# Optimization experiments

Measured on AMD Instinct MI355X. Metric: run time of the kernel, lower is better.

The kernel has to match this reference:

```python
import jax, jax.numpy as jnp
import numpy as np

B, T, E = 4, 2048, 256
H = 8
HD = E // H
FE = 4
L = 4
EPS = 1e-5


def _layernorm(x, g, b):
    mu = jnp.mean(x, axis=-1, keepdims=True)
    var = jnp.mean((x - mu) ** 2, axis=-1, keepdims=True)
    return (x - mu) * jax.lax.rsqrt(var + EPS) * g + b


def setup_inputs() -> dict:
    key = jax.random.key(0)
    ks = jax.random.split(key, 14)
    s = 0.02
    inp = {
        "x": jax.random.normal(ks[0], (B, T, E), dtype=jnp.float32),
        "qkv_w": jax.random.normal(ks[1], (L, E, 3 * E), dtype=jnp.float32) * s,
        "qkv_b": jnp.zeros((L, 3 * E), jnp.float32),
        "out_w": jax.random.normal(ks[2], (L, E, E), dtype=jnp.float32) * s,
        "out_b": jnp.zeros((L, E), jnp.float32),
        "ff1_w": jax.random.normal(ks[3], (L, E, FE * E), dtype=jnp.float32) * s,
        "ff1_b": jnp.zeros((L, FE * E), jnp.float32),
        "ff2_w": jax.random.normal(ks[4], (L, FE * E, E), dtype=jnp.float32) * s,
        "ff2_b": jnp.zeros((L, E), jnp.float32),
        "ln1_g": jnp.ones((L, E), jnp.float32),
        "ln1_b": jnp.zeros((L, E), jnp.float32),
        "ln2_g": jnp.ones((L, E), jnp.float32),
        "ln2_b": jnp.zeros((L, E), jnp.float32),
    }
    return inp


def _fourier_pe(x):
    # freqs over even indices: 10000^(-i/E), i = 0,2,...,E-2  -> E/2 freqs
    freqs = jnp.power(10000.0, -jnp.arange(0, E, 2, dtype=jnp.float32) / E)
    pos = jnp.arange(T, dtype=jnp.float32)[:, None]          # (T,1)
    sinusoid = pos * freqs[None, :]                            # (T, E/2)
    pe = jnp.concatenate([jnp.sin(sinusoid), jnp.cos(sinusoid)], axis=-1)  # (T,E)
    return x + pe[None, :, :]


def _forward(x, qkv_w, qkv_b, out_w, out_b, ff1_w, ff1_b, ff2_w, ff2_b,
             ln1_g, ln1_b, ln2_g, ln2_b):
    x = _fourier_pe(x)
    scale = 1.0 / np.sqrt(HD)
    for i in range(L):
        # attention (dropout = identity at eval)
        qkv = x @ qkv_w[i] + qkv_b[i]                          # (B,T,3E)
        qkv = qkv.reshape(B, T, H, 3, HD)                      # chunk of 3*hd -> (3,hd)
        q, k, v = qkv[..., 0, :], qkv[..., 1, :], qkv[..., 2, :]  # (B,T,H,HD)
        scores = jnp.einsum("bqhd,bkhd->bhqk", q, k) * scale   # (B,H,T,T)
        w = jax.nn.softmax(scores, axis=-1)
        attn = jnp.einsum("bhqk,bkhd->bqhd", w, v).reshape(B, T, E)
        attn = attn @ out_w[i] + out_b[i]
        x = _layernorm(x + attn, ln1_g[i], ln1_b[i])
        # feedforward
        h = jax.nn.relu(x @ ff1_w[i] + ff1_b[i])
        ff = h @ ff2_w[i] + ff2_b[i]
        x = _layernorm(x + ff, ln2_g[i], ln2_b[i])
    return x


def reference(x, qkv_w, qkv_b, out_w, out_b, ff1_w, ff1_b, ff2_w, ff2_b,
              ln1_g, ln1_b, ln2_g, ln2_b):
    return _forward(x, qkv_w, qkv_b, out_w, out_b, ff1_w, ff1_b, ff2_w, ff2_b,
                    ln1_g, ln1_b, ln2_g, ln2_b)
```

## Files before the change

### kernel.cpp

```cpp
#include <hip/hip_runtime.h>
#include <hip/hip_bf16.h>
#include <stdint.h>

typedef unsigned short u16;
typedef _Float16 f16;
typedef short vs8 __attribute__((ext_vector_type(8)));
typedef float vf4 __attribute__((ext_vector_type(4)));
typedef _Float16 vh2 __attribute__((ext_vector_type(2)));
typedef _Float16 vh4 __attribute__((ext_vector_type(4)));
typedef _Float16 vh8 __attribute__((ext_vector_type(8)));
typedef __fp16 hw2 __attribute__((ext_vector_type(2)));



__device__ __forceinline__ void gload16(const u16* g, u16* l) {
  __builtin_amdgcn_global_load_lds((const __attribute__((address_space(1))) void*)g,
                                   (__attribute__((address_space(3))) void*)l,
                                   16, 0, 0);
}

__device__ __forceinline__ float fexp2(float x) {
#if __has_builtin(__builtin_amdgcn_exp2f)
  return __builtin_amdgcn_exp2f(x);
#else
  return __expf(x * 0.69314718056f);
#endif
}

__global__ void pe_kernel(const float* __restrict__ x, __hip_bfloat16* __restrict__ Xb) {
  int gid = blockIdx.x * 256 + threadIdx.x;
  int row = gid >> 6;
  int e0 = (gid & 63) * 4;
  int t = row & 2047;
  int f0 = (e0 < 128) ? e0 : (e0 - 128);
  const float c = -13.287712379549449f / 128.0f;
  const float inv2pi = 0.15915494309189535f;
  float4 xv = *(const float4*)(x + (size_t)row * 256 + e0);
  u16 o[4];
#pragma unroll
  for (int j = 0; j < 4; ++j) {
    float freq = fexp2(c * (float)(f0 + j));
    float rev = (float)t * freq * inv2pi;
    rev = rev - floorf(rev);
    float pe = (e0 < 128) ? __builtin_amdgcn_sinf(rev) : __builtin_amdgcn_cosf(rev);
    float xin = (j == 0) ? xv.x : (j == 1) ? xv.y : (j == 2) ? xv.z : xv.w;
    __hip_bfloat16 hb = __float2bfloat16(xin + pe);
    o[j] = *(u16*)&hb;
  }
  *(uint2*)((u16*)Xb + (size_t)row * 256 + e0) = *(uint2*)o;
}

__global__ void transpose_cast_all(
    const float* __restrict__ w0, const float* __restrict__ w1,
    const float* __restrict__ w2, const float* __restrict__ w3,
    u16* __restrict__ o0, u16* __restrict__ o1,
    u16* __restrict__ o2, u16* __restrict__ o3) {
  __shared__ float tile[32][33];
  int flat = blockIdx.x;
  int layer = flat / 768;
  int r = flat - layer * 768;
  const float* ip; u16* op; int K, N, kt, nt;
  if (r < 192)      {              ip = w0; op = o0; K = 256;  N = 768;  kt = r & 7;  nt = r >> 3; }
  else if (r < 256) { int q=r-192; ip = w1; op = o1; K = 256;  N = 256;  kt = q & 7;  nt = q >> 3; }
  else if (r < 512) { int q=r-256; ip = w2; op = o2; K = 256;  N = 1024; kt = q & 7;  nt = q >> 3; }
  else              { int q=r-512; ip = w3; op = o3; K = 1024; N = 256;  kt = q & 31; nt = q >> 5; }
  ip += (size_t)layer * K * N;
  op += (size_t)layer * N * K;
  int k0 = kt * 32, n0 = nt * 32;
  int tx = threadIdx.x, ty = threadIdx.y;
#pragma unroll
  for (int rr = 0; rr < 4; ++rr) {
    int k = ty + rr * 8;
    tile[k][tx] = ip[(size_t)(k0 + k) * N + (n0 + tx)];
  }
  __syncthreads();
#pragma unroll
  for (int rr = 0; rr < 4; ++rr) {
    int n = ty + rr * 8;
    __hip_bfloat16 v = __float2bfloat16(tile[tx][n]);
    op[(size_t)(n0 + n) * K + (k0 + tx)] = *(u16*)&v;
  }
}

__global__ __launch_bounds__(256, 2) void gemm_relu(
    const u16* __restrict__ A, const u16* __restrict__ Bt,
    const float* __restrict__ bias, __hip_bfloat16* __restrict__ outB,
    int M, int N, int K) {
  __shared__ u16 As[128 * 64];
  __shared__ u16 Bs[128 * 64];
  int tid = threadIdx.x;
  int wave = tid >> 6, lane = tid & 63;
  int wm = wave & 1, wn = wave >> 1;
  int m0 = blockIdx.y * 128, n0 = blockIdx.x * 128;
  int lr = lane & 15, lq = lane >> 4;
  int swz = (lr & 7) << 3;

  vf4 acc[4][4];
#pragma unroll
  for (int i = 0; i < 4; ++i)
#pragma unroll
    for (int j = 0; j < 4; ++j) {
      acc[i][j][0] = 0.f; acc[i][j][1] = 0.f; acc[i][j][2] = 0.f; acc[i][j][3] = 0.f;
    }

  int srow = tid >> 3;
  int sc = (tid & 7) * 8;
  int cswz = (((tid & 7) ^ (srow & 7)) * 8);
  const u16* ag = A + (size_t)(m0 + srow) * K + cswz;
  const u16* bg = Bt + (size_t)(n0 + srow) * K + cswz;
  u16* al = As + srow * 64 + sc;
  u16* bl = Bs + srow * 64 + sc;
  const size_t rstride32 = (size_t)32 * K;

  for (int k0 = 0; k0 < K; k0 += 64) {
#pragma unroll
    for (int r = 0; r < 4; ++r) {
      gload16(ag + k0 + r * rstride32, al + r * 32 * 64);
      gload16(bg + k0 + r * rstride32, bl + r * 32 * 64);
    }
    __syncthreads();
#pragma unroll
    for (int kk = 0; kk < 2; ++kk) {
      vs8 av[4], bv[4];
#pragma unroll
      for (int i = 0; i < 4; ++i)
        av[i] = *(const vs8*)&As[(wm * 64 + i * 16 + lr) * 64 + ((kk * 32 + lq * 8) ^ swz)];
#pragma unroll
      for (int j = 0; j < 4; ++j)
        bv[j] = *(const vs8*)&Bs[(wn * 64 + j * 16 + lr) * 64 + ((kk * 32 + lq * 8) ^ swz)];
#pragma unroll
      for (int i = 0; i < 4; ++i)
#pragma unroll
        for (int j = 0; j < 4; ++j)
          acc[i][j] = __builtin_amdgcn_mfma_f32_16x16x32_bf16(av[i], bv[j], acc[i][j], 0, 0, 0);
    }
    __syncthreads();
  }

#pragma unroll
  for (int i = 0; i < 4; ++i) {
    int row0 = m0 + wm * 64 + i * 16 + lq * 4;
#pragma unroll
    for (int j = 0; j < 4; ++j) {
      int col = n0 + wn * 64 + j * 16 + lr;
      float bb = bias[col];
#pragma unroll
      for (int r = 0; r < 4; ++r) {
        size_t idx = (size_t)(row0 + r) * N + col;
        outB[idx] = __float2bfloat16(fmaxf(acc[i][j][r] + bb, 0.0f));
      }
    }
  }
}

__global__ __launch_bounds__(256, 3) void gemm_qkv64(
    const u16* __restrict__ A, const u16* __restrict__ Bt,
    const float* __restrict__ bias, f16* __restrict__ outH,
    int M, int N, int K) {
  __shared__ u16 As[64 * 64];
  __shared__ u16 Bs[128 * 64];
  int tid = threadIdx.x;
  int wave = tid >> 6, lane = tid & 63;
  int wm = wave & 1, wn = wave >> 1;
  int m0 = blockIdx.y * 64, n0 = blockIdx.x * 128;
  int lr = lane & 15, lq = lane >> 4;
  int swz = (lr & 7) << 3;

  vf4 acc[2][4];
#pragma unroll
  for (int i = 0; i < 2; ++i)
#pragma unroll
    for (int j = 0; j < 4; ++j) { acc[i][j][0]=0.f; acc[i][j][1]=0.f; acc[i][j][2]=0.f; acc[i][j][3]=0.f; }

  int srow = tid >> 3;
  int sc = (tid & 7) * 8;
  int cswz = (((tid & 7) ^ (srow & 7)) * 8);
  const u16* ag = A + (size_t)(m0 + srow) * K + cswz;
  const u16* bg = Bt + (size_t)(n0 + srow) * K + cswz;
  u16* al = As + srow * 64 + sc;
  u16* bl = Bs + srow * 64 + sc;
  const size_t rstride32 = (size_t)32 * K;

  for (int k0 = 0; k0 < K; k0 += 64) {
#pragma unroll
    for (int r = 0; r < 2; ++r)
      gload16(ag + k0 + r * rstride32, al + r * 32 * 64);
#pragma unroll
    for (int r = 0; r < 4; ++r)
      gload16(bg + k0 + r * rstride32, bl + r * 32 * 64);
    __syncthreads();
#pragma unroll
    for (int kk = 0; kk < 2; ++kk) {
      vs8 av[2], bv[4];
#pragma unroll
      for (int i = 0; i < 2; ++i)
        av[i] = *(const vs8*)&As[(wm * 32 + i * 16 + lr) * 64 + ((kk * 32 + lq * 8) ^ swz)];
#pragma unroll
      for (int j = 0; j < 4; ++j)
        bv[j] = *(const vs8*)&Bs[(wn * 64 + j * 16 + lr) * 64 + ((kk * 32 + lq * 8) ^ swz)];
#pragma unroll
      for (int i = 0; i < 2; ++i)
#pragma unroll
        for (int j = 0; j < 4; ++j)
          acc[i][j] = __builtin_amdgcn_mfma_f32_16x16x32_bf16(av[i], bv[j], acc[i][j], 0, 0, 0);
    }
    __syncthreads();
  }

#pragma unroll
  for (int i = 0; i < 2; ++i) {
    int row0 = m0 + wm * 32 + i * 16 + lq * 4;
#pragma unroll
    for (int j = 0; j < 4; ++j) {
      int col = n0 + wn * 64 + j * 16 + lr;
      float bb = bias[col];
#pragma unroll
      for (int r = 0; r < 4; ++r)
        outH[(size_t)(row0 + r) * N + col] = (f16)(acc[i][j][r] + bb);
    }
  }
}

__global__ __launch_bounds__(512, 2) void gemm_ln(
    const u16* __restrict__ A, const u16* __restrict__ Bt,
    const float* __restrict__ bias, const __hip_bfloat16* __restrict__ res,
    const float* __restrict__ gam, const float* __restrict__ bet,
    __hip_bfloat16* __restrict__ outB, float* __restrict__ outF, int K,
    const f16* __restrict__ OfA, const float* __restrict__ lf) {
  __shared__ u16 As[32 * 64];
  __shared__ u16 Bs[256 * 64];
  __shared__ float ps[4][32], ps2[4][32], mur[32], rsr[32];
  __shared__ float invs[8][32];
  int tid = threadIdx.x;
  int wave = tid >> 6, lane = tid & 63;
  int wm = wave & 1, wn = wave >> 1;
  int lr = lane & 15, lq = lane >> 4;
  int m0 = blockIdx.x * 32;
  int swz = (lr & 7) << 3;

  vf4 acc[4];
#pragma unroll
  for (int j = 0; j < 4; ++j) { acc[j][0]=0.f; acc[j][1]=0.f; acc[j][2]=0.f; acc[j][3]=0.f; }

  int sr = tid >> 3;
  int sc = (tid & 7) * 8;
  int cswz = (((tid & 7) ^ (sr & 7)) * 8);
  const u16* ag = A + (size_t)(m0 + sr) * K + cswz;
  const u16* bg = Bt + (size_t)sr * K + cswz;
  u16* al = As + sr * 64 + sc;
  u16* bl = Bs + sr * 64 + sc;

  if (OfA) {
    if (tid < 256) {
      int h = tid >> 5, rl = tid & 31;
      int row = m0 + rl, bb_ = row >> 11, t = row & 2047;
      int g = bb_ * 8 + h;
      invs[h][rl] = 1.0f / (lf[g * 2048 + t] + lf[65536 + g * 2048 + t]);
    }
    __syncthreads();
  }

  for (int k0 = 0; k0 < K; k0 += 64) {
    if (tid < 256) {
      if (OfA) {
        size_t off = (size_t)(m0 + sr) * 256 + k0 + cswz;
        vh8 a0 = *(const vh8*)(OfA + off);
        vh8 a1 = *(const vh8*)(OfA + 2097152 + off);
        float inv = invs[(k0 + cswz) >> 5][sr];
        union { vs8 v; u16 u[8]; } pk;
#pragma unroll
        for (int j = 0; j < 8; ++j) {
          __hip_bfloat16 hb = __float2bfloat16(((float)a0[j] + (float)a1[j]) * inv);
          pk.u[j] = *(u16*)&hb;
        }
        *(vs8*)al = pk.v;
      } else {
        gload16(ag + k0, al);
      }
    }
#pragma unroll
    for (int r = 0; r < 4; ++r)
      gload16(bg + k0 + (size_t)(r * 64) * K, bl + r * 64 * 64);
    __syncthreads();
#pragma unroll
    for (int kk = 0; kk < 2; ++kk) {
      vs8 av, bv[4];
      av = *(const vs8*)&As[(wm * 16 + lr) * 64 + ((kk * 32 + lq * 8) ^ swz)];
#pragma unroll
      for (int j = 0; j < 4; ++j)
        bv[j] = *(const vs8*)&Bs[(wn * 64 + j * 16 + lr) * 64 + ((kk * 32 + lq * 8) ^ swz)];
#pragma unroll
      for (int j = 0; j < 4; ++j)
        acc[j] = __builtin_amdgcn_mfma_f32_16x16x32_bf16(av, bv[j], acc[j], 0, 0, 0);
    }
    __syncthreads();
  }

  float sum_[4], sq_[4];
#pragma unroll
  for (int r = 0; r < 4; ++r) { sum_[r] = 0.f; sq_[r] = 0.f; }
#pragma unroll
  for (int j = 0; j < 4; ++j) {
    int col = wn * 64 + j * 16 + lr;
    float bb = bias[col];
#pragma unroll
    for (int r = 0; r < 4; ++r) {
      int row = m0 + wm * 16 + lq * 4 + r;
      float v = acc[j][r] + bb + __bfloat162float(res[(size_t)row * 256 + col]);
      acc[j][r] = v;
      sum_[r] += v;
      sq_[r] += v * v;
    }
  }
#pragma unroll
  for (int r = 0; r < 4; ++r) {
#pragma unroll
    for (int m = 1; m <= 8; m <<= 1) {
      sum_[r] += __shfl_xor(sum_[r], m);
      sq_[r]  += __shfl_xor(sq_[r], m);
    }
  }
  if (lr == 0) {
#pragma unroll
    for (int r = 0; r < 4; ++r) {
      int rl = wm * 16 + lq * 4 + r;
      ps[wn][rl] = sum_[r];
      ps2[wn][rl] = sq_[r];
    }
  }
  __syncthreads();
  if (tid < 32) {
    float s = ps[0][tid] + ps[1][tid] + ps[2][tid] + ps[3][tid];
    float s2 = ps2[0][tid] + ps2[1][tid] + ps2[2][tid] + ps2[3][tid];
    float mu = s * (1.0f / 256.0f);
    float var = s2 * (1.0f / 256.0f) - mu * mu;
    mur[tid] = mu;
    rsr[tid] = rsqrtf(var + 1e-5f);
  }
  __syncthreads();
#pragma unroll
  for (int r = 0; r < 4; ++r) {
    int rl = wm * 16 + lq * 4 + r;
    float mu = mur[rl], rs = rsr[rl];
    int row = m0 + rl;
#pragma unroll
    for (int j = 0; j < 4; ++j) {
      int col = wn * 64 + j * 16 + lr;
      float o = (acc[j][r] - mu) * rs * gam[col] + bet[col];
      size_t idx = (size_t)row * 256 + col;
      outB[idx] = __float2bfloat16(o);
      if (outF) outF[idx] = o;
    }
  }
}

__global__ __launch_bounds__(512, 4) void attn_mfma(const f16* __restrict__ qkv,
                                                    f16* __restrict__ Of,
                                                    float* __restrict__ lf) {
  __shared__ __align__(16) u16 lds[2][9344];
  int tid = threadIdx.x;
  int wave = tid >> 6, lane = tid & 63;
  int lr = lane & 15, quad = lane >> 4;

  int id = blockIdx.x;
  int xcd = id & 7, slot = id >> 3;
  int grp = xcd * 4 + (slot & 3);
  int qt = (slot >> 2) & 7;
  int split = slot >> 5;
  int b = grp >> 3, h = grp & 7;
  int q0 = qt * 256;
  int kv0 = split << 10;
  int rowbase = b * 2048;
  const f16* base_bh = qkv + (size_t)rowbase * 768 + h * 96;

  vh8 qf[2];
#pragma unroll
  for (int nt = 0; nt < 2; ++nt) {
    int qr = q0 + wave * 32 + nt * 16 + lr;
    vh8 t = *(const vh8*)(base_bh + (size_t)qr * 768 + quad * 8);
#pragma unroll
    for (int j = 0; j < 8; ++j) t[j] = t[j] * (f16)0.25508682f;
    qf[nt] = t;
  }

  vf4 O[2][2], lO[2];
#pragma unroll
  for (int a = 0; a < 2; ++a) {
    lO[a][0]=0.f; lO[a][1]=0.f; lO[a][2]=0.f; lO[a][3]=0.f;
#pragma unroll
    for (int d = 0; d < 2; ++d) { O[a][d][0]=0.f; O[a][d][1]=0.f; O[a][d][2]=0.f; O[a][d][3]=0.f; }
  }

  int srK = tid >> 2;
  int scK = (tid & 3) * 8;
  const f16* kg = base_bh + (size_t)(kv0 + srK) * 768 + 32 + scK;
  int kvp = tid >> 3;
  int d4 = (tid & 7) * 4;
  const f16* vg = base_bh + (size_t)(kv0 + kvp * 2) * 768 + 64 + d4;

  const vf4 z4 = {0.f, 0.f, 0.f, 0.f};
  const vh4 onesh = {(f16)1.0f, (f16)1.0f, (f16)1.0f, (f16)1.0f};
  const size_t cstep = (size_t)128 * 768;

  {
    vh8 k0 = *(const vh8*)kg;
    *(vh8*)&lds[0][srK * 40 + scK] = k0;
    vh4 a = *(const vh4*)vg;
    vh4 bb = *(const vh4*)(vg + 768);
    f16* vt0 = (f16*)&lds[0][5120];
#pragma unroll
    for (int i = 0; i < 4; ++i) {
      vh2 pr; pr[0] = a[i]; pr[1] = bb[i];
      *(vh2*)(vt0 + (d4 + i) * 132 + kvp * 2) = pr;
    }
  }
  __syncthreads();

  for (int c = 0; c < 8; ++c) {
    int cur = c & 1;
    const f16* Ks = (const f16*)&lds[cur][0];
    const f16* VT = (const f16*)&lds[cur][5120];

    vh8 kn; vh4 va, vb;
    if (c < 7) {
      kn = *(const vh8*)(kg + (size_t)(c + 1) * cstep);
      const f16* vp = vg + (size_t)(c + 1) * cstep;
      va = *(const vh4*)vp;
      vb = *(const vh4*)(vp + 768);
    }

    __builtin_amdgcn_s_setprio(1);
#pragma unroll
    for (int t16 = 0; t16 < 8; ++t16) {
      vh8 ak = *(const vh8*)&Ks[(t16 * 16 + lr) * 40 + quad * 8];
      vf4 s0 = __builtin_amdgcn_mfma_f32_16x16x32_f16(ak, qf[0], z4, 0, 0, 0);
      vf4 s1 = __builtin_amdgcn_mfma_f32_16x16x32_f16(ak, qf[1], z4, 0, 0, 0);
      vh4 p0, p1;
      ((hw2*)&p0)[0] = __builtin_amdgcn_cvt_pkrtz(fexp2(s0[0]), fexp2(s0[1]));
      ((hw2*)&p0)[1] = __builtin_amdgcn_cvt_pkrtz(fexp2(s0[2]), fexp2(s0[3]));
      ((hw2*)&p1)[0] = __builtin_amdgcn_cvt_pkrtz(fexp2(s1[0]), fexp2(s1[1]));
      ((hw2*)&p1)[1] = __builtin_amdgcn_cvt_pkrtz(fexp2(s1[2]), fexp2(s1[3]));
      vh4 vf0 = *(const vh4*)&VT[(0 * 16 + lr) * 132 + t16 * 16 + quad * 4];
      vh4 vf1 = *(const vh4*)&VT[(1 * 16 + lr) * 132 + t16 * 16 + quad * 4];
      O[0][0] = __builtin_amdgcn_mfma_f32_16x16x16f16(p0, vf0, O[0][0], 0, 0, 0);
      O[0][1] = __builtin_amdgcn_mfma_f32_16x16x16f16(p0, vf1, O[0][1], 0, 0, 0);
      O[1][0] = __builtin_amdgcn_mfma_f32_16x16x16f16(p1, vf0, O[1][0], 0, 0, 0);
      O[1][1] = __builtin_amdgcn_mfma_f32_16x16x16f16(p1, vf1, O[1][1], 0, 0, 0);
      lO[0] = __builtin_amdgcn_mfma_f32_16x16x16f16(p0, onesh, lO[0], 0, 0, 0);
      lO[1] = __builtin_amdgcn_mfma_f32_16x16x16f16(p1, onesh, lO[1], 0, 0, 0);
    }
    __builtin_amdgcn_s_setprio(0);

    if (c < 7) {
      *(vh8*)&lds[cur ^ 1][srK * 40 + scK] = kn;
      f16* vt1 = (f16*)&lds[cur ^ 1][5120];
#pragma unroll
      for (int i = 0; i < 4; ++i) {
        vh2 pr; pr[0] = va[i]; pr[1] = vb[i];
        *(vh2*)(vt1 + (d4 + i) * 132 + kvp * 2) = pr;
      }
    }
    __syncthreads();
  }

#pragma unroll
  for (int nt = 0; nt < 2; ++nt) {
#pragma unroll
    for (int r = 0; r < 4; ++r) {
      int tq = q0 + wave * 32 + nt * 16 + quad * 4 + r;
      if (lr == 0) lf[split * 65536 + grp * 2048 + tq] = lO[nt][r];
      int row = rowbase + tq;
#pragma unroll
      for (int dt = 0; dt < 2; ++dt) {
        int col = h * 32 + dt * 16 + lr;
        Of[(size_t)split * 2097152 + (size_t)row * 256 + col] = (f16)O[nt][dt][r];
      }
    }
  }
}

extern "C" void kernel_launch(void* const* d_in, const int* in_sizes, int n_in,
                              void* d_out, int out_size, void* d_ws, size_t ws_size,
                              hipStream_t stream) {
  (void)in_sizes; (void)n_in; (void)out_size; (void)ws_size;
  const float* x     = (const float*)d_in[0];
  const float* qkv_b = (const float*)d_in[2];
  const float* out_b = (const float*)d_in[4];
  const float* ff1_b = (const float*)d_in[6];
  const float* ff2_b = (const float*)d_in[8];
  const float* ln1_g = (const float*)d_in[9];
  const float* ln1_b = (const float*)d_in[10];
  const float* ln2_g = (const float*)d_in[11];
  const float* ln2_b = (const float*)d_in[12];

  char* ws = (char*)d_ws;
  f16*            Of    = (f16*)(ws + 0);
  __hip_bfloat16* Xb    = (__hip_bfloat16*)(ws + 8388608);
  float*          lf    = (float*)(ws + 12582912);
  f16*            qkvH  = (f16*)(ws + 25165824);
  __hip_bfloat16* hB    = (__hip_bfloat16*)(ws + 20971520);
  u16* qkvwT = (u16*)(ws + 37748736);
  u16* outwT = (u16*)(ws + 39321600);
  u16* ff1wT = (u16*)(ws + 39845888);
  u16* ff2wT = (u16*)(ws + 41943040);

  pe_kernel<<<2048, 256, 0, stream>>>(x, Xb);
  transpose_cast_all<<<3072, dim3(32, 8), 0, stream>>>(
      (const float*)d_in[1], (const float*)d_in[3], (const float*)d_in[5], (const float*)d_in[7],
      qkvwT, outwT, ff1wT, ff2wT);

  for (int l = 0; l < 4; ++l) {
    gemm_qkv64<<<dim3(6, 128), 256, 0, stream>>>((const u16*)Xb, qkvwT + (size_t)l * 768 * 256,
        qkv_b + l * 768, qkvH, 8192, 768, 256);
    attn_mfma<<<512, 512, 0, stream>>>(qkvH, Of, lf);
    gemm_ln<<<256, 512, 0, stream>>>(nullptr, outwT + (size_t)l * 256 * 256,
        out_b + l * 256, Xb, ln1_g + l * 256, ln1_b + l * 256, Xb, nullptr, 256, Of, lf);
    gemm_relu<<<dim3(8, 64), 256, 0, stream>>>((const u16*)Xb, ff1wT + (size_t)l * 1024 * 256,
        ff1_b + l * 1024, hB, 8192, 1024, 256);
    float* lnout = (l == 3) ? (float*)d_out : nullptr;
    gemm_ln<<<256, 512, 0, stream>>>((const u16*)hB, ff2wT + (size_t)l * 256 * 1024,
        ff2_b + l * 256, Xb, ln2_g + l * 256, ln2_b + l * 256, Xb, lnout, 1024, nullptr, nullptr);
  }
}
```

Measured before the change: 401.9 us.

## Double-buffer gemm_ln K-loop with 32-wide stages and register prefetch of A

The gemm_ln K-loop becomes a double-buffered pipeline with 32-wide K stages. The next stage's A and B tiles are issued via global_load_lds, and the attention-output A operand is prefetched into registers two stages ahead, with manual s_waitcnt and raw s_barrier instead of __syncthreads. A new 4-byte LDS load path and a new XOR swizzle for 32-column tiles are added. The aim is to hide global load latency behind MFMA work, at the cost of more barriers per K, fragile hand-written waitcnt counts and smaller MFMA batches per stage.

```diff
diff --git a/kernel.cpp b/kernel.cpp
--- a/kernel.cpp
+++ b/kernel.cpp
@@ -12,11 +12,15 @@
 typedef __fp16 hw2 __attribute__((ext_vector_type(2)));
 
 
-
 __device__ __forceinline__ void gload16(const u16* g, u16* l) {
   __builtin_amdgcn_global_load_lds((const __attribute__((address_space(1))) void*)g,
                                    (__attribute__((address_space(3))) void*)l,
                                    16, 0, 0);
+}
+__device__ __forceinline__ void gload4(const u16* g, u16* l) {
+  __builtin_amdgcn_global_load_lds((const __attribute__((address_space(1))) void*)g,
+                                   (__attribute__((address_space(3))) void*)l,
+                                   4, 0, 0);
 }
 
 __device__ __forceinline__ float fexp2(float x) {
@@ -227,8 +231,8 @@
     const float* __restrict__ gam, const float* __restrict__ bet,
     __hip_bfloat16* __restrict__ outB, float* __restrict__ outF, int K,
     const f16* __restrict__ OfA, const float* __restrict__ lf) {
-  __shared__ u16 As[32 * 64];
-  __shared__ u16 Bs[256 * 64];
+  __shared__ u16 As[2][32 * 32];
+  __shared__ u16 Bs[2][256 * 32];
   __shared__ float ps[4][32], ps2[4][32], mur[32], rsr[32];
   __shared__ float invs[8][32];
   int tid = threadIdx.x;
@@ -236,64 +240,107 @@
   int wm = wave & 1, wn = wave >> 1;
   int lr = lane & 15, lq = lane >> 4;
   int m0 = blockIdx.x * 32;
-  int swz = (lr & 7) << 3;
+  int fsw = (lq * 8) ^ ((lr & 3) << 3);
 
   vf4 acc[4];
 #pragma unroll
   for (int j = 0; j < 4; ++j) { acc[j][0]=0.f; acc[j][1]=0.f; acc[j][2]=0.f; acc[j][3]=0.f; }
 
-  int sr = tid >> 3;
-  int sc = (tid & 7) * 8;
-  int cswz = (((tid & 7) ^ (sr & 7)) * 8);
-  const u16* ag = A + (size_t)(m0 + sr) * K + cswz;
-  const u16* bg = Bt + (size_t)sr * K + cswz;
-  u16* al = As + sr * 64 + sc;
-  u16* bl = Bs + sr * 64 + sc;
+  int sr0 = tid >> 2, g = tid & 3;
+  int colB = g * 8;
+  int colBs = (g ^ (sr0 & 3)) * 8;
+  const u16* bg = Bt + (size_t)sr0 * K + colBs;
+  int rowA = tid >> 4;
+  int colA2 = (tid & 15) * 2;
+  int colAs = colA2 ^ ((rowA & 3) << 3);
+  const u16* ag4 = A + (size_t)(m0 + rowA) * K + colAs;
+  const size_t OfS = 2097152;
 
   if (OfA) {
     if (tid < 256) {
       int h = tid >> 5, rl = tid & 31;
       int row = m0 + rl, bb_ = row >> 11, t = row & 2047;
-      int g = bb_ * 8 + h;
-      invs[h][rl] = 1.0f / (lf[g * 2048 + t] + lf[65536 + g * 2048 + t]);
+      int gg = bb_ * 8 + h;
+      invs[h][rl] = 1.0f / (lf[gg * 2048 + t] + lf[65536 + gg * 2048 + t]);
     }
     __syncthreads();
   }
 
-  for (int k0 = 0; k0 < K; k0 += 64) {
-    if (tid < 256) {
+  int NS = K >> 5;
+  vh8 ra0, ra1;
+
+  if (OfA) {
+    if (tid < 128) {
+      size_t off = (size_t)(m0 + sr0) * 256 + colBs;
+      vh8 a0 = *(const vh8*)(OfA + off);
+      vh8 a1 = *(const vh8*)(OfA + OfS + off);
+      float inv = invs[colBs >> 5][sr0];
+      union { vs8 v; u16 u[8]; } pk;
+#pragma unroll
+      for (int j = 0; j < 8; ++j) {
+        __hip_bfloat16 hb = __float2bfloat16(((float)a0[j] + (float)a1[j]) * inv);
+        pk.u[j] = *(u16*)&hb;
+      }
+      *(vs8*)&As[0][sr0 * 32 + colB] = pk.v;
+    }
+    gload16(bg, &Bs[0][sr0 * 32 + colB]);
+    gload16(bg + (size_t)128 * K, &Bs[0][(sr0 + 128) * 32 + colB]);
+    if (tid < 128 && NS > 1) {
+      size_t off = (size_t)(m0 + sr0) * 256 + 32 + colBs;
+      ra0 = *(const vh8*)(OfA + off);
+      ra1 = *(const vh8*)(OfA + OfS + off);
+    }
+    asm volatile("s_waitcnt lgkmcnt(0)" ::: "memory");
+  } else {
+    gload4(ag4, &As[0][tid * 2]);
+    gload16(bg, &Bs[0][sr0 * 32 + colB]);
+    gload16(bg + (size_t)128 * K, &Bs[0][(sr0 + 128) * 32 + colB]);
+  }
+
+  for (int s = 0; s < NS; ++s) {
+    int cur = s & 1;
+    if (s + 1 < NS) {
+      int k1 = (s + 1) << 5;
+      u16* bl = &Bs[cur ^ 1][sr0 * 32 + colB];
+      if (!OfA) gload4(ag4 + k1, &As[cur ^ 1][tid * 2]);
+      gload16(bg + k1, bl);
+      gload16(bg + k1 + (size_t)128 * K, bl + 128 * 32);
       if (OfA) {
-        size_t off = (size_t)(m0 + sr) * 256 + k0 + cswz;
-        vh8 a0 = *(const vh8*)(OfA + off);
-        vh8 a1 = *(const vh8*)(OfA + 2097152 + off);
-        float inv = invs[(k0 + cswz) >> 5][sr];
-        union { vs8 v; u16 u[8]; } pk;
-#pragma unroll
-        for (int j = 0; j < 8; ++j) {
-          __hip_bfloat16 hb = __float2bfloat16(((float)a0[j] + (float)a1[j]) * inv);
-          pk.u[j] = *(u16*)&hb;
+        if (tid < 128) {
+          float inv = invs[k1 >> 5][sr0];
+          union { vs8 v; u16 u[8]; } pk;
+#pragma unroll
+          for (int j = 0; j < 8; ++j) {
+            __hip_bfloat16 hb = __float2bfloat16(((float)ra0[j] + (float)ra1[j]) * inv);
+            pk.u[j] = *(u16*)&hb;
+          }
+          *(vs8*)&As[cur ^ 1][sr0 * 32 + colB] = pk.v;
         }
-        *(vs8*)al = pk.v;
+        asm volatile("s_waitcnt vmcnt(2)" ::: "memory");
+        asm volatile("s_waitcnt lgkmcnt(0)" ::: "memory");
       } else {
-        gload16(ag + k0, al);
+        asm volatile("s_waitcnt vmcnt(3)" ::: "memory");
       }
-    }
-#pragma unroll
-    for (int r = 0; r < 4; ++r)
-      gload16(bg + k0 + (size_t)(r * 64) * K, bl + r * 64 * 64);
-    __syncthreads();
-#pragma unroll
-    for (int kk = 0; kk < 2; ++kk) {
-      vs8 av, bv[4];
-      av = *(const vs8*)&As[(wm * 16 + lr) * 64 + ((kk * 32 + lq * 8) ^ swz)];
-#pragma unroll
-      for (int j = 0; j < 4; ++j)
-        bv[j] = *(const vs8*)&Bs[(wn * 64 + j * 16 + lr) * 64 + ((kk * 32 + lq * 8) ^ swz)];
-#pragma unroll
-      for (int j = 0; j < 4; ++j)
-        acc[j] = __builtin_amdgcn_mfma_f32_16x16x32_bf16(av, bv[j], acc[j], 0, 0, 0);
-    }
-    __syncthreads();
+    } else {
+      asm volatile("s_waitcnt vmcnt(0)" ::: "memory");
+      if (OfA) asm volatile("s_waitcnt lgkmcnt(0)" ::: "memory");
+    }
+    __builtin_amdgcn_s_barrier();
+    __builtin_amdgcn_sched_barrier(0);
+    if (OfA && tid < 128 && s + 2 < NS) {
+      size_t off = (size_t)(m0 + sr0) * 256 + (size_t)((s + 2) << 5) + colBs;
+      ra0 = *(const vh8*)(OfA + off);
+      ra1 = *(const vh8*)(OfA + OfS + off);
+    }
+    vs8 av = *(const vs8*)&As[cur][(wm * 16 + lr) * 32 + fsw];
+    vs8 bv[4];
+#pragma unroll
+    for (int j = 0; j < 4; ++j)
+      bv[j] = *(const vs8*)&Bs[cur][(wn * 64 + j * 16 + lr) * 32 + fsw];
+#pragma unroll
+    for (int j = 0; j < 4; ++j)
+      acc[j] = __builtin_amdgcn_mfma_f32_16x16x32_bf16(av, bv[j], acc[j], 0, 0, 0);
+    __builtin_amdgcn_s_barrier();
   }
 
   float sum_[4], sq_[4];
```

Measured after the change: 435.3 us. +8.3%, slower.

## Fuse FF1 and next-layer QKV GEMMs into the LayerNorm GEMM epilogues

Applied to the files above, without the earlier changes.

The LayerNorm output tile is kept in shared memory, and the following GEMM is run inside the same kernel. After LN1 it computes FF1 with ReLU, and after LN2 it computes the next layer's QKV projection. This removes the separate gemm_relu and per-layer gemm_qkv launches, along with the activation re-read from global memory. The cost is that the fused second GEMM runs on only 256 blocks of 32 rows and 512 threads, without double buffering. The extra shared memory (about 50KB more) may also lower occupancy.

```diff
diff --git a/kernel.cpp b/kernel.cpp
--- a/kernel.cpp
+++ b/kernel.cpp
@@ -10,7 +10,6 @@
 typedef _Float16 vh4 __attribute__((ext_vector_type(4)));
 typedef _Float16 vh8 __attribute__((ext_vector_type(8)));
 typedef __fp16 hw2 __attribute__((ext_vector_type(2)));
-
 
 
 __device__ __forceinline__ void gload16(const u16* g, u16* l) {
@@ -82,77 +81,6 @@
   }
 }
 
-__global__ __launch_bounds__(256, 2) void gemm_relu(
-    const u16* __restrict__ A, const u16* __restrict__ Bt,
-    const float* __restrict__ bias, __hip_bfloat16* __restrict__ outB,
-    int M, int N, int K) {
-  __shared__ u16 As[128 * 64];
-  __shared__ u16 Bs[128 * 64];
-  int tid = threadIdx.x;
-  int wave = tid >> 6, lane = tid & 63;
-  int wm = wave & 1, wn = wave >> 1;
-  int m0 = blockIdx.y * 128, n0 = blockIdx.x * 128;
-  int lr = lane & 15, lq = lane >> 4;
-  int swz = (lr & 7) << 3;
-
-  vf4 acc[4][4];
-#pragma unroll
-  for (int i = 0; i < 4; ++i)
-#pragma unroll
-    for (int j = 0; j < 4; ++j) {
-      acc[i][j][0] = 0.f; acc[i][j][1] = 0.f; acc[i][j][2] = 0.f; acc[i][j][3] = 0.f;
-    }
-
-  int srow = tid >> 3;
-  int sc = (tid & 7) * 8;
-  int cswz = (((tid & 7) ^ (srow & 7)) * 8);
-  const u16* ag = A + (size_t)(m0 + srow) * K + cswz;
-  const u16* bg = Bt + (size_t)(n0 + srow) * K + cswz;
-  u16* al = As + srow * 64 + sc;
-  u16* bl = Bs + srow * 64 + sc;
-  const size_t rstride32 = (size_t)32 * K;
-
-  for (int k0 = 0; k0 < K; k0 += 64) {
-#pragma unroll
-    for (int r = 0; r < 4; ++r) {
-      gload16(ag + k0 + r * rstride32, al + r * 32 * 64);
-      gload16(bg + k0 + r * rstride32, bl + r * 32 * 64);
-    }
-    __syncthreads();
-#pragma unroll
-    for (int kk = 0; kk < 2; ++kk) {
-      vs8 av[4], bv[4];
-#pragma unroll
-      for (int i = 0; i < 4; ++i)
-        av[i] = *(const vs8*)&As[(wm * 64 + i * 16 + lr) * 64 + ((kk * 32 + lq * 8) ^ swz)];
-#pragma unroll
-      for (int j = 0; j < 4; ++j)
-        bv[j] = *(const vs8*)&Bs[(wn * 64 + j * 16 + lr) * 64 + ((kk * 32 + lq * 8) ^ swz)];
-#pragma unroll
-      for (int i = 0; i < 4; ++i)
-#pragma unroll
-        for (int j = 0; j < 4; ++j)
-          acc[i][j] = __builtin_amdgcn_mfma_f32_16x16x32_bf16(av[i], bv[j], acc[i][j], 0, 0, 0);
-    }
-    __syncthreads();
-  }
-
-#pragma unroll
-  for (int i = 0; i < 4; ++i) {
-    int row0 = m0 + wm * 64 + i * 16 + lq * 4;
-#pragma unroll
-    for (int j = 0; j < 4; ++j) {
-      int col = n0 + wn * 64 + j * 16 + lr;
-      float bb = bias[col];
-#pragma unroll
-      for (int r = 0; r < 4; ++r) {
-        size_t idx = (size_t)(row0 + r) * N + col;
-        outB[idx] = __float2bfloat16(fmaxf(acc[i][j][r] + bb, 0.0f));
-      }
-    }
-  }
-}
-
 __global__ __launch_bounds__(256, 3) void gemm_qkv64(
     const u16* __restrict__ A, const u16* __restrict__ Bt,
     const float* __restrict__ bias, f16* __restrict__ outH,
@@ -221,14 +149,18 @@
   }
 }
 
-__global__ __launch_bounds__(512, 2) void gemm_ln(
+__global__ __launch_bounds__(512, 2) void gemm_ln2(
     const u16* __restrict__ A, const u16* __restrict__ Bt,
     const float* __restrict__ bias, const __hip_bfloat16* __restrict__ res,
     const float* __restrict__ gam, const float* __restrict__ bet,
     __hip_bfloat16* __restrict__ outB, float* __restrict__ outF, int K,
-    const f16* __restrict__ OfA, const float* __restrict__ lf) {
+    const f16* __restrict__ OfA, const float* __restrict__ lf,
+    const u16* __restrict__ Bt2, const float* __restrict__ bias2, int N2,
+    __hip_bfloat16* __restrict__ out2B, f16* __restrict__ out2H) {
   __shared__ u16 As[32 * 64];
   __shared__ u16 Bs[256 * 64];
+  __shared__ u16 As2[32 * 256];
+  __shared__ u16 Bs2[256 * 64];
   __shared__ float ps[4][32], ps2[4][32], mur[32], rsr[32];
   __shared__ float invs[8][32];
   int tid = threadIdx.x;
@@ -348,8 +280,54 @@
       int col = wn * 64 + j * 16 + lr;
       float o = (acc[j][r] - mu) * rs * gam[col] + bet[col];
       size_t idx = (size_t)row * 256 + col;
-      outB[idx] = __float2bfloat16(o);
+      __hip_bfloat16 ob = __float2bfloat16(o);
+      outB[idx] = ob;
       if (outF) outF[idx] = o;
+      if (N2) As2[rl * 256 + (col ^ ((rl & 7) << 3))] = *(u16*)&ob;
+    }
+  }
+
+  if (N2 > 0) {
+    __syncthreads();
+    int rowb = tid >> 3, cgb = tid & 7;
+    int cswzb = ((cgb ^ (rowb & 7)) * 8);
+    const u16* bg2 = Bt2 + (size_t)rowb * 256 + cswzb;
+    u16* bl2 = Bs2 + rowb * 64 + cgb * 8;
+    int nch = N2 >> 8;
+    for (int nc = 0; nc < nch; ++nc) {
+      vf4 a2[4];
+#pragma unroll
+      for (int j = 0; j < 4; ++j) { a2[j][0]=0.f; a2[j][1]=0.f; a2[j][2]=0.f; a2[j][3]=0.f; }
+#pragma unroll
+      for (int ks = 0; ks < 4; ++ks) {
+#pragma unroll
+        for (int i = 0; i < 4; ++i)
+          gload16(bg2 + (size_t)(nc * 256 + i * 64) * 256 + ks * 64, bl2 + i * 64 * 64);
+        __syncthreads();
+#pragma unroll
+        for (int kk = 0; kk < 2; ++kk) {
+          vs8 av2 = *(const vs8*)&As2[(wm * 16 + lr) * 256 + ((ks * 64 + kk * 32 + lq * 8) ^ swz)];
+          vs8 bv;
+#pragma unroll
+          for (int j = 0; j < 4; ++j) {
+            bv = *(const vs8*)&Bs2[(wn * 64 + j * 16 + lr) * 64 + ((kk * 32 + lq * 8) ^ swz)];
+            a2[j] = __builtin_amdgcn_mfma_f32_16x16x32_bf16(av2, bv, a2[j], 0, 0, 0);
+          }
+        }
+        __syncthreads();
+      }
+#pragma unroll
+      for (int j = 0; j < 4; ++j) {
+        int col = nc * 256 + wn * 64 + j * 16 + lr;
+        float bb2 = bias2[col];
+#pragma unroll
+        for (int r = 0; r < 4; ++r) {
+          int row = m0 + wm * 16 + lq * 4 + r;
+          float v = a2[j][r] + bb2;
+          if (out2H) out2H[(size_t)row * N2 + col] = (f16)v;
+          else       out2B[(size_t)row * N2 + col] = __float2bfloat16(fmaxf(v, 0.0f));
+        }
+      }
     }
   }
 }
@@ -497,28 +475,32 @@
   f16*            Of    = (f16*)(ws + 0);
   __hip_bfloat16* Xb    = (__hip_bfloat16*)(ws + 8388608);
   float*          lf    = (float*)(ws + 12582912);
-  f16*            qkvH  = (f16*)(ws + 25165824);
-  __hip_bfloat16* hB    = (__hip_bfloat16*)(ws + 20971520);
-  u16* qkvwT = (u16*)(ws + 37748736);
-  u16* outwT = (u16*)(ws + 39321600);
-  u16* ff1wT = (u16*)(ws + 39845888);
-  u16* ff2wT = (u16*)(ws + 41943040);
+  f16*            qkvH  = (f16*)(ws + 16777216);
+  __hip_bfloat16* hB    = (__hip_bfloat16*)(ws + 29360128);
+  u16* qkvwT = (u16*)(ws + 46137344);
+  u16* outwT = (u16*)(ws + 47710208);
+  u16* ff1wT = (u16*)(ws + 48234496);
+  u16* ff2wT = (u16*)(ws + 50331648);
 
   pe_kernel<<<2048, 256, 0, stream>>>(x, Xb);
   transpose_cast_all<<<3072, dim3(32, 8), 0, stream>>>(
       (const float*)d_in[1], (const float*)d_in[3], (const float*)d_in[5], (const float*)d_in[7],
       qkvwT, outwT, ff1wT, ff2wT);
 
+  gemm_qkv64<<<dim3(6, 128), 256, 0, stream>>>((const u16*)Xb, qkvwT,
+      qkv_b, qkvH, 8192, 768, 256);
+
   for (int l = 0; l < 4; ++l) {
-    gemm_qkv64<<<dim3(6, 128), 256, 0, stream>>>((const u16*)Xb, qkvwT + (size_t)l * 768 * 256,
-        qkv_b + l * 768, qkvH, 8192, 768, 256);
     attn_mfma<<<512, 512, 0, stream>>>(qkvH, Of, lf);
-    gemm_ln<<<256, 512, 0, stream>>>(nullptr, outwT + (size_t)l * 256 * 256,
-        out_b + l * 256, Xb, ln1_g + l * 256, ln1_b + l * 256, Xb, nullptr, 256, Of, lf);
-    gemm_relu<<<dim3(8, 64), 256, 0, stream>>>((const u16*)Xb, ff1wT + (size_t)l * 1024 * 256,
-        ff1_b + l * 1024, hB, 8192, 1024, 256);
+    gemm_ln2<<<256, 512, 0, stream>>>(nullptr, outwT + (size_t)l * 256 * 256,
+        out_b + l * 256, Xb, ln1_g + l * 256, ln1_b + l * 256, Xb, nullptr, 256, Of, lf,
+        ff1wT + (size_t)l * 1024 * 256, ff1_b + l * 1024, 1024, hB, nullptr);
     float* lnout = (l == 3) ? (float*)d_out : nullptr;
-    gemm_ln<<<256, 512, 0, stream>>>((const u16*)hB, ff2wT + (size_t)l * 256 * 1024,
-        ff2_b + l * 256, Xb, ln2_g + l * 256, ln2_b + l * 256, Xb, lnout, 1024, nullptr, nullptr);
-  }
-}
+    const u16* nqw = (l < 3) ? (qkvwT + (size_t)(l + 1) * 768 * 256) : nullptr;
+    const float* nqb = (l < 3) ? (qkv_b + (l + 1) * 768) : qkv_b;
+    int n2 = (l < 3) ? 768 : 0;
+    gemm_ln2<<<256, 512, 0, stream>>>((const u16*)hB, ff2wT + (size_t)l * 256 * 1024,
+        ff2_b + l * 256, Xb, ln2_g + l * 256, ln2_b + l * 256, Xb, lnout, 1024, nullptr, nullptr,
+        nqw, nqb, n2, nullptr, qkvH);
+  }
+}
```

Result: slower. 438.0 us (+9.0%).
